# Kernel tuning notes

Hardware: AMD Instinct MI355X
Metric: run time of the kernel (lower is better)

## Reference

```python
import jax, jax.numpy as jnp
import numpy as np

N_NODES = 100000
N_EDGES = 3200000
F_IN = 128
F_OUT = 128


def setup_inputs() -> dict:
    key = jax.random.key(0)
    k_x, k_r, k_c, k_v, k_w = jax.random.split(key, 5)
    x = jax.random.normal(k_x, (N_NODES, F_IN), dtype=jnp.float32)
    adj_rows = jnp.sort(jax.random.randint(k_r, (N_EDGES,), 0, N_NODES, dtype=jnp.int32))
    adj_cols = jax.random.randint(k_c, (N_EDGES,), 0, N_NODES, dtype=jnp.int32)
    adj_vals = jax.random.uniform(k_v, (N_EDGES,), dtype=jnp.float32)
    # glorot init for W, zeros for bias (as in the original module)
    limit = np.sqrt(6.0 / (F_IN + F_OUT)).astype(np.float32)
    W = jax.random.uniform(k_w, (F_IN, F_OUT), dtype=jnp.float32, minval=-limit, maxval=limit)
    b = jnp.zeros((F_OUT,), dtype=jnp.float32)
    return {"x": x, "adj_rows": adj_rows, "adj_cols": adj_cols,
            "adj_vals": adj_vals, "W": W, "b": b}


def reference(x, adj_rows, adj_cols, adj_vals, W, b):
    # dropout = 0.0 (disabled), sparse_inputs = False, featureless = False
    # pre_sup = x @ W  -- dense feature transform [N, F_out]
    pre_sup = jnp.matmul(x, W)
    # support @ pre_sup -- sparse adjacency SpMM via gather + segment_sum
    msgs = adj_vals[:, None] * pre_sup[adj_cols]        # [E, F_out]
    agg = jax.ops.segment_sum(msgs, adj_rows,
                              num_segments=N_NODES,
                              indices_are_sorted=True)   # [N, F_out]
    out = agg + b
    return jax.nn.relu(out)
```

## Files before the change

kernel.cpp:

```cpp
#include <hip/hip_runtime.h>
#include <cstdint>
#include <cstddef>

#define N_NODES 100000
#define N_EDGES 3200000
#define F_IN 128
#define F_OUT 128

#define ROWPTR_BYTES ((N_NODES + 1) * 4)
#define O_XB   (((ROWPTR_BYTES) + 255) & ~255)
#define XB_BYTES (N_NODES * F_IN * 2)
#define O_WT   (O_XB + XB_BYTES)
#define WT_BYTES (F_OUT * F_IN * 2)
#define NEED_A ((size_t)(O_WT + WT_BYTES))

typedef __attribute__((ext_vector_type(8))) short short8;
typedef __attribute__((ext_vector_type(4))) float f32x4;

__device__ __forceinline__ unsigned short f2bf(float f) {
    union { float f; unsigned u; } v; v.f = f;
    return (unsigned short)((v.u + 0x7FFFu + ((v.u >> 16) & 1u)) >> 16);
}
__device__ __forceinline__ float bflo(unsigned u) {
    union { unsigned u; float f; } v; v.u = u << 16; return v.f;
}
__device__ __forceinline__ float bfhi(unsigned u) {
    union { unsigned u; float f; } v; v.u = u & 0xFFFF0000u; return v.f;
}

__device__ __forceinline__ int lower_bound_i32(const int* __restrict__ a, int n, int key) {
    int lo = 0, hi = n;
    while (lo < hi) {
        int mid = (lo + hi) >> 1;
        if (a[mid] < key) lo = mid + 1; else hi = mid;
    }
    return lo;
}

__global__ __launch_bounds__(256) void prep_kernel(
    const float*    __restrict__ x4_,
    const int*      __restrict__ rows,
    const float*    __restrict__ W,
    int*            __restrict__ rowptr,
    uint2*          __restrict__ xb2,
    unsigned short* __restrict__ Wt)
{
    const unsigned g = blockIdx.x * 256 + threadIdx.x;
    const float4* __restrict__ x4 = (const float4*)x4_;

    if (g < (N_NODES * F_IN / 4)) {
        const float4 a = x4[g];
        uint2 p;
        p.x = (unsigned)f2bf(a.x) | ((unsigned)f2bf(a.y) << 16);
        p.y = (unsigned)f2bf(a.z) | ((unsigned)f2bf(a.w) << 16);
        xb2[g] = p;
    }
    if (g <= N_NODES)
        rowptr[g] = lower_bound_i32(rows, N_EDGES, g);
    if (g < F_IN * F_OUT) {
        const int c = g >> 7, k = g & 127;
        Wt[g] = f2bf(W[k * F_OUT + c]);
    }
}

__global__ __launch_bounds__(256) void fused_spmm_gemm(
    const unsigned*       __restrict__ xb,
    const int*            __restrict__ cols,
    const float*          __restrict__ vals,
    const int*            __restrict__ rowptr,
    const unsigned short* __restrict__ Wt,
    const float*          __restrict__ bias,
    float*                __restrict__ out)
{
    __shared__ char A_lds[64 * 256];

    const int t    = threadIdx.x;
    const int lane = t & 63;
    const int w    = t >> 6;
    const int r0   = blockIdx.x * 64;

    for (int i = 0; i < 16; ++i) {
        const int lrow = w * 16 + i;
        const int row  = r0 + lrow;
        float ax = 0.f, ay = 0.f;
        if (row < N_NODES) {
            const int e0 = rowptr[row], e1 = rowptr[row + 1];
            int e = e0;
            for (; e + 16 <= e1; e += 16) {
                int c[16]; float v[16]; unsigned u[16];
                #pragma unroll
                for (int j = 0; j < 16; ++j) { c[j] = cols[e + j]; v[j] = vals[e + j]; }
                #pragma unroll
                for (int j = 0; j < 16; ++j) u[j] = xb[(unsigned)c[j] * 64u + lane];
                #pragma unroll
                for (int j = 0; j < 16; ++j) {
                    ax = fmaf(v[j], bflo(u[j]), ax);
                    ay = fmaf(v[j], bfhi(u[j]), ay);
                }
            }
            for (; e + 4 <= e1; e += 4) {
                int c[4]; float v[4]; unsigned u[4];
                #pragma unroll
                for (int j = 0; j < 4; ++j) { c[j] = cols[e + j]; v[j] = vals[e + j]; }
                #pragma unroll
                for (int j = 0; j < 4; ++j) u[j] = xb[(unsigned)c[j] * 64u + lane];
                #pragma unroll
                for (int j = 0; j < 4; ++j) {
                    ax = fmaf(v[j], bflo(u[j]), ax);
                    ay = fmaf(v[j], bfhi(u[j]), ay);
                }
            }
            for (; e < e1; ++e) {
                const float v = vals[e];
                const unsigned u = xb[(unsigned)cols[e] * 64u + lane];
                ax = fmaf(v, bflo(u), ax);
                ay = fmaf(v, bfhi(u), ay);
            }
        }
        const unsigned p = (unsigned)f2bf(ax) | ((unsigned)f2bf(ay) << 16);
        *reinterpret_cast<unsigned*>(
            A_lds + lrow * 256 + ((lane * 4) ^ ((lrow & 7) << 4))) = p;
    }
    __syncthreads();

    const int lr = lane & 15;
    const int lg = lane >> 4;
    const int swA = (lr & 7) << 4;

    const short* __restrict__ Wbase =
        reinterpret_cast<const short*>(Wt) + lr * F_IN + lg * 8;
    const char* Abase = A_lds + (w * 16 + lr) * 256;

    f32x4 acc[8];
    #pragma unroll
    for (int n = 0; n < 8; ++n) acc[n] = (f32x4){0.f, 0.f, 0.f, 0.f};

    #pragma unroll
    for (int ks = 0; ks < 4; ++ks) {
        const short8 a = *reinterpret_cast<const short8*>(
            Abase + ((ks * 64 + lg * 16) ^ swA));
        #pragma unroll
        for (int n = 0; n < 8; ++n) {
            const short8 b = *reinterpret_cast<const short8*>(
                Wbase + n * 16 * F_IN + ks * 32);
            acc[n] = __builtin_amdgcn_mfma_f32_16x16x32_bf16(a, b, acc[n], 0, 0, 0);
        }
    }

    const int row_base = r0 + w * 16 + lg * 4;
    #pragma unroll
    for (int n = 0; n < 8; ++n) {
        const int col = n * 16 + lr;
        const float bb = bias[col];
        #pragma unroll
        for (int reg = 0; reg < 4; ++reg) {
            const int r = row_base + reg;
            if (r < N_NODES)
                out[(size_t)r * F_OUT + col] = fmaxf(acc[n][reg] + bb, 0.f);
        }
    }
}

__global__ __launch_bounds__(256) void spmm_ax_fallback(
    const float* __restrict__ x,
    const int*   __restrict__ rows,
    const int*   __restrict__ cols,
    const float* __restrict__ vals,
    float*       __restrict__ out)
{
    const int row  = blockIdx.x * 4 + (threadIdx.x >> 6);
    const int lane = threadIdx.x & 63;
    if (row >= N_NODES) return;
    const int e0 = lower_bound_i32(rows, N_EDGES, row);
    const int e1 = lower_bound_i32(rows, N_EDGES, row + 1);
    const float2* __restrict__ x2 = reinterpret_cast<const float2*>(x);
    float ax = 0.f, ay = 0.f;
    int e = e0;
    for (; e + 8 <= e1; e += 8) {
        int c[8]; float v[8]; float2 a[8];
        #pragma unroll
        for (int j = 0; j < 8; ++j) { c[j] = cols[e + j]; v[j] = vals[e + j]; }
        #pragma unroll
        for (int j = 0; j < 8; ++j) a[j] = x2[(unsigned)c[j] * 64u + lane];
        #pragma unroll
        for (int j = 0; j < 8; ++j) {
            ax = fmaf(v[j], a[j].x, ax); ay = fmaf(v[j], a[j].y, ay);
        }
    }
    for (; e < e1; ++e) {
        const float v = vals[e];
        const float2 a = x2[(unsigned)cols[e] * 64u + lane];
        ax = fmaf(v, a.x, ax); ay = fmaf(v, a.y, ay);
    }
    float2 o; o.x = ax; o.y = ay;
    reinterpret_cast<float2*>(out)[(size_t)row * 64 + lane] = o;
}

__global__ __launch_bounds__(256) void gemm_inplace_fallback(
    float*       __restrict__ out,
    const float* __restrict__ W,
    const float* __restrict__ bias)
{
    __shared__ short A_lds[64][136];
    __shared__ short Wt_lds[F_OUT][136];
    const int t  = threadIdx.x;
    const int r0 = blockIdx.x * 64;
    const int rows_here = (N_NODES - r0 < 64) ? (N_NODES - r0) : 64;
    {
        const float4* __restrict__ A4 =
            reinterpret_cast<const float4*>(out + (size_t)r0 * F_IN);
        const int nA = rows_here * 32;
        for (int i = t; i < nA; i += 256) {
            const int r = i >> 5, q = i & 31;
            const float4 va = A4[i];
            uint2 p;
            p.x = (unsigned)f2bf(va.x) | ((unsigned)f2bf(va.y) << 16);
            p.y = (unsigned)f2bf(va.z) | ((unsigned)f2bf(va.w) << 16);
            *reinterpret_cast<uint2*>(&A_lds[r][q * 4]) = p;
        }
    }
    if (t < F_OUT)
        for (int k = 0; k < F_IN; ++k)
            Wt_lds[t][k] = (short)f2bf(W[k * F_OUT + t]);
    __syncthreads();

    const int lane = t & 63, w = t >> 6, lr = lane & 15, lg = lane >> 4;
    f32x4 acc[8];
    #pragma unroll
    for (int n = 0; n < 8; ++n) acc[n] = (f32x4){0.f, 0.f, 0.f, 0.f};
    #pragma unroll
    for (int ks = 0; ks < 4; ++ks) {
        const short8 a = *reinterpret_cast<const short8*>(
            &A_lds[w * 16 + lr][ks * 32 + lg * 8]);
        #pragma unroll
        for (int n = 0; n < 8; ++n) {
            const short8 b = *reinterpret_cast<const short8*>(
                &Wt_lds[n * 16 + lr][ks * 32 + lg * 8]);
            acc[n] = __builtin_amdgcn_mfma_f32_16x16x32_bf16(a, b, acc[n], 0, 0, 0);
        }
    }
    const int row_base = r0 + w * 16 + lg * 4;
    #pragma unroll
    for (int n = 0; n < 8; ++n) {
        const int col = n * 16 + lr;
        const float bb = bias[col];
        #pragma unroll
        for (int reg = 0; reg < 4; ++reg) {
            const int r = row_base + reg;
            if (r < N_NODES)
                out[(size_t)r * F_OUT + col] = fmaxf(acc[n][reg] + bb, 0.f);
        }
    }
}

extern "C" void kernel_launch(void* const* d_in, const int* in_sizes, int n_in,
                              void* d_out, int out_size, void* d_ws, size_t ws_size,
                              hipStream_t stream) {
    const float* x    = (const float*)d_in[0];
    const int*   rows = (const int*)  d_in[1];
    const int*   cols = (const int*)  d_in[2];
    const float* vals = (const float*)d_in[3];
    const float* W    = (const float*)d_in[4];
    const float* b    = (const float*)d_in[5];
    float* out = (float*)d_out;
    char*  ws  = (char*)d_ws;

    if (ws_size >= NEED_A) {
        int*            rowptr = (int*)ws;
        unsigned short* xb     = (unsigned short*)(ws + O_XB);
        unsigned short* Wt     = (unsigned short*)(ws + O_WT);
        prep_kernel<<<(N_NODES * F_IN / 4 + 255) / 256, 256, 0, stream>>>(
            x, rows, W, rowptr, (uint2*)xb, Wt);
        fused_spmm_gemm<<<(N_NODES + 63) / 64, 256, 0, stream>>>(
            (const unsigned*)xb, cols, vals, rowptr, Wt, b, out);
    } else {
        spmm_ax_fallback<<<(N_NODES + 3) / 4, 256, 0, stream>>>(
            x, rows, cols, vals, out);
        gemm_inplace_fallback<<<(N_NODES + 63) / 64, 256, 0, stream>>>(out, W, b);
    }
}
```

Before: 319.5 us.

## Use 1024-thread blocks for fused SpMM-GEMM and split prep kernel

```diff
diff --git a/kernel.cpp b/kernel.cpp
--- a/kernel.cpp
+++ b/kernel.cpp
@@ -37,17 +37,10 @@
     return lo;
 }
 
-__global__ __launch_bounds__(256) void prep_kernel(
-    const float*    __restrict__ x4_,
-    const int*      __restrict__ rows,
-    const float*    __restrict__ W,
-    int*            __restrict__ rowptr,
-    uint2*          __restrict__ xb2,
-    unsigned short* __restrict__ Wt)
+__global__ __launch_bounds__(256) void convert_x_kernel(
+    const float4* __restrict__ x4, uint2* __restrict__ xb2)
 {
     const unsigned g = blockIdx.x * 256 + threadIdx.x;
-    const float4* __restrict__ x4 = (const float4*)x4_;
-
     if (g < (N_NODES * F_IN / 4)) {
         const float4 a = x4[g];
         uint2 p;
@@ -55,6 +48,15 @@
         p.y = (unsigned)f2bf(a.z) | ((unsigned)f2bf(a.w) << 16);
         xb2[g] = p;
     }
+}
+
+__global__ __launch_bounds__(256) void aux_kernel(
+    const int*      __restrict__ rows,
+    const float*    __restrict__ W,
+    int*            __restrict__ rowptr,
+    unsigned short* __restrict__ Wt)
+{
+    const unsigned g = blockIdx.x * 256 + threadIdx.x;
     if (g <= N_NODES)
         rowptr[g] = lower_bound_i32(rows, N_EDGES, g);
     if (g < F_IN * F_OUT) {
@@ -63,7 +65,7 @@
     }
 }
 
-__global__ __launch_bounds__(256) void fused_spmm_gemm(
+__global__ __launch_bounds__(1024, 8) void fused_spmm_gemm(
     const unsigned*       __restrict__ xb,
     const int*            __restrict__ cols,
     const float*          __restrict__ vals,
@@ -79,8 +81,8 @@
     const int w    = t >> 6;
     const int r0   = blockIdx.x * 64;
 
-    for (int i = 0; i < 16; ++i) {
-        const int lrow = w * 16 + i;
+    for (int i = 0; i < 4; ++i) {
+        const int lrow = w * 4 + i;
         const int row  = r0 + lrow;
         float ax = 0.f, ay = 0.f;
         if (row < N_NODES) {
@@ -123,40 +125,41 @@
     }
     __syncthreads();
 
+    const int rt = w & 3;
+    const int cg = w >> 2;
     const int lr = lane & 15;
     const int lg = lane >> 4;
     const int swA = (lr & 7) << 4;
 
-    const short* __restrict__ Wbase =
-        reinterpret_cast<const short*>(Wt) + lr * F_IN + lg * 8;
-    const char* Abase = A_lds + (w * 16 + lr) * 256;
-
-    f32x4 acc[8];
-    #pragma unroll
-    for (int n = 0; n < 8; ++n) acc[n] = (f32x4){0.f, 0.f, 0.f, 0.f};
+    const char* Abase = A_lds + (rt * 16 + lr) * 256;
+
+    f32x4 acc[2];
+    acc[0] = (f32x4){0.f, 0.f, 0.f, 0.f};
+    acc[1] = (f32x4){0.f, 0.f, 0.f, 0.f};
 
     #pragma unroll
     for (int ks = 0; ks < 4; ++ks) {
         const short8 a = *reinterpret_cast<const short8*>(
             Abase + ((ks * 64 + lg * 16) ^ swA));
         #pragma unroll
-        for (int n = 0; n < 8; ++n) {
+        for (int nn = 0; nn < 2; ++nn) {
             const short8 b = *reinterpret_cast<const short8*>(
-                Wbase + n * 16 * F_IN + ks * 32);
-            acc[n] = __builtin_amdgcn_mfma_f32_16x16x32_bf16(a, b, acc[n], 0, 0, 0);
-        }
-    }
-
-    const int row_base = r0 + w * 16 + lg * 4;
-    #pragma unroll
-    for (int n = 0; n < 8; ++n) {
-        const int col = n * 16 + lr;
+                reinterpret_cast<const short*>(Wt) +
+                (cg * 32 + nn * 16 + lr) * F_IN + lg * 8 + ks * 32);
+            acc[nn] = __builtin_amdgcn_mfma_f32_16x16x32_bf16(a, b, acc[nn], 0, 0, 0);
+        }
+    }
+
+    const int row_base = r0 + rt * 16 + lg * 4;
+    #pragma unroll
+    for (int nn = 0; nn < 2; ++nn) {
+        const int col = cg * 32 + nn * 16 + lr;
         const float bb = bias[col];
         #pragma unroll
         for (int reg = 0; reg < 4; ++reg) {
             const int r = row_base + reg;
             if (r < N_NODES)
-                out[(size_t)r * F_OUT + col] = fmaxf(acc[n][reg] + bb, 0.f);
+                out[(size_t)r * F_OUT + col] = fmaxf(acc[nn][reg] + bb, 0.f);
         }
     }
 }
@@ -269,9 +272,10 @@
         int*            rowptr = (int*)ws;
         unsigned short* xb     = (unsigned short*)(ws + O_XB);
         unsigned short* Wt     = (unsigned short*)(ws + O_WT);
-        prep_kernel<<<(N_NODES * F_IN / 4 + 255) / 256, 256, 0, stream>>>(
-            x, rows, W, rowptr, (uint2*)xb, Wt);
-        fused_spmm_gemm<<<(N_NODES + 63) / 64, 256, 0, stream>>>(
+        convert_x_kernel<<<(N_NODES * F_IN / 4 + 255) / 256, 256, 0, stream>>>(
+            (const float4*)x, (uint2*)xb);
+        aux_kernel<<<(N_NODES + 256) / 256, 256, 0, stream>>>(rows, W, rowptr, Wt);
+        fused_spmm_gemm<<<(N_NODES + 63) / 64, 1024, 0, stream>>>(
             (const unsigned*)xb, cols, vals, rowptr, Wt, b, out);
     } else {
         spmm_ax_fallback<<<(N_NODES + 3) / 4, 256, 0, stream>>>(
```

Result: faster. 291.5 us (-8.8%).
